# Performance work log

Measured on AMD Instinct MI355X. Metric: run time of the kernel, lower is better.

Reference implementation:

```python
import jax, jax.numpy as jnp
import numpy as np

N, E = 100000, 1280000
IN_D, FEAT, HID, OUT = 256, 64, 64, 64
NEG_SLOPE = 0.2


def _gat_conv(x, src, dst, w, a_s, a_d, b, n):
    # x: [N, in], w: [in, out], a_s/a_d/b: [out]; edges src->dst (messages flow to dst)
    h = x @ w                                   # [N, out]
    e = jax.nn.leaky_relu((h @ a_s)[src] + (h @ a_d)[dst], NEG_SLOPE)  # [E]
    m = jax.ops.segment_max(e, dst, num_segments=n)                     # scatter-softmax (stable)
    ex = jnp.exp(e - m[dst])
    den = jax.ops.segment_sum(ex, dst, num_segments=n)
    alpha = ex / (den[dst] + 1e-16)
    out = jax.ops.segment_sum(alpha[:, None] * h[src], dst, num_segments=n)
    return out + b


def setup_inputs() -> dict:
    key = jax.random.key(0)
    ks = jax.random.split(key, 16)
    rn = lambda k, shape, s=0.05: jax.random.normal(k, shape, jnp.float32) * s
    return {
        'x': jax.random.normal(ks[0], (N, IN_D), jnp.float32),
        'src': jax.random.randint(ks[1], (E,), 0, N),
        'dst': jax.random.randint(ks[2], (E,), 0, N),
        'lin_w': rn(ks[3], (IN_D, FEAT)), 'lin_b': jnp.zeros((FEAT,), jnp.float32),
        'w1': rn(ks[4], (FEAT, HID)), 'a1s': rn(ks[5], (HID,)), 'a1d': rn(ks[6], (HID,)), 'b1': jnp.zeros((HID,), jnp.float32),
        'w2': rn(ks[7], (HID, HID)), 'a2s': rn(ks[8], (HID,)), 'a2d': rn(ks[9], (HID,)), 'b2': jnp.zeros((HID,), jnp.float32),
        'w3': rn(ks[10], (HID, OUT)), 'a3s': rn(ks[11], (OUT,)), 'a3d': rn(ks[12], (OUT,)), 'b3': jnp.zeros((OUT,), jnp.float32),
    }


def reference(x, src, dst, lin_w, lin_b, w1, a1s, a1d, b1, w2, a2s, a2d, b2, w3, a3s, a3d, b3):
    n = x.shape[0]
    loop = jnp.arange(n, dtype=src.dtype)        # GATConv add_self_loops=True
    s = jnp.concatenate([src, loop])
    d = jnp.concatenate([dst, loop])
    h = x @ lin_w + lin_b                        # feature_pre linear
    h = jax.nn.relu(_gat_conv(h, s, d, w1, a1s, a1d, b1, n))  # dropout is identity in eval
    h = jax.nn.relu(_gat_conv(h, s, d, w2, a2s, a2d, b2, n))
    h = _gat_conv(h, s, d, w3, a3s, a3d, b3, n)
    norm = jnp.linalg.norm(h, axis=-1, keepdims=True)          # F.normalize(p=2, dim=-1)
    return h / jnp.maximum(norm, 1e-12)
```

## Files before the change

### kernel.cpp

```cpp
#include <hip/hip_runtime.h>


constexpr float NEG_SLOPE = 0.2f;
#define BKT_SHIFT 9
#define BKT_N     512
#define PCHUNK    2048
#define SRC_BITS  17

typedef __attribute__((ext_vector_type(8))) short bf16x8;
typedef __attribute__((ext_vector_type(4))) float f32x4;

__device__ inline ushort f2bf(float x) {
    union { float f; uint u; } v; v.f = x;
    return (ushort)((v.u + 0x7FFFu + ((v.u >> 16) & 1u)) >> 16);
}
__device__ inline void bf2f(uint u, float& lo, float& hi) {
    union { uint u; float f; } a, b;
    a.u = u << 16; b.u = u & 0xFFFF0000u;
    lo = a.f; hi = b.f;
}
__device__ inline uint pk(float a, float b) {
    return (uint)f2bf(a) | ((uint)f2bf(b) << 16);
}

__global__ __launch_bounds__(256) void prep_w(
    const float* __restrict__ lw, const float* __restrict__ w1,
    const float* __restrict__ w2, const float* __restrict__ w3,
    ushort* __restrict__ lwT, ushort* __restrict__ w1T,
    ushort* __restrict__ w2T, ushort* __restrict__ w3T,
    int* __restrict__ cnt, int* __restrict__ ticket, int n)
{
    const int i = blockIdx.x * 256 + threadIdx.x;
    if (i < n) cnt[i] = 0;
    if (i == 0) *ticket = 0;
    if (i < 64 * 256) {
        const int nn = i >> 8, k = i & 255;
        lwT[i] = f2bf(lw[k * 64 + nn]);
    } else {
        const int j = i - 64 * 256;
        if (j < 4096) {
            const int nn = j >> 6, k = j & 63;
            w1T[j] = f2bf(w1[k * 64 + nn]);
            w2T[j] = f2bf(w2[k * 64 + nn]);
            w3T[j] = f2bf(w3[k * 64 + nn]);
        }
    }
}

__global__ __launch_bounds__(256) void gemm_pre(
    const float* __restrict__ x, const ushort* __restrict__ lwT,
    const float* __restrict__ bias, ushort* __restrict__ C, int M)
{
    __shared__ __align__(16) ushort ctile[4][16][64];
    const int tid = threadIdx.x;
    const int w = tid >> 6, lane = tid & 63;
    const int rw0 = (blockIdx.x * 4 + w) * 16;
    if (rw0 >= M) return;
    const int c = lane & 15, q = lane >> 4;

    const float* ap = x + (size_t)(rw0 + c) * 256 + q * 8;
    float4 pv[16];
    #pragma unroll
    for (int s = 0; s < 8; ++s) {
        pv[2 * s]     = *(const float4*)(ap + s * 32);
        pv[2 * s + 1] = *(const float4*)(ap + s * 32 + 4);
    }

    f32x4 acc[4];
    #pragma unroll
    for (int t = 0; t < 4; ++t) acc[t] = (f32x4){0.f, 0.f, 0.f, 0.f};

    #pragma unroll
    for (int s = 0; s < 8; ++s) {
        const float4 p0 = pv[2 * s];
        const float4 p1 = pv[2 * s + 1];
        bf16x8 af;
        af[0] = (short)f2bf(p0.x); af[1] = (short)f2bf(p0.y);
        af[2] = (short)f2bf(p0.z); af[3] = (short)f2bf(p0.w);
        af[4] = (short)f2bf(p1.x); af[5] = (short)f2bf(p1.y);
        af[6] = (short)f2bf(p1.z); af[7] = (short)f2bf(p1.w);
        #pragma unroll
        for (int t = 0; t < 4; ++t) {
            const bf16x8 bf = *(const bf16x8*)(lwT + (size_t)(t * 16 + c) * 256 + s * 32 + q * 8);
            acc[t] = __builtin_amdgcn_mfma_f32_16x16x32_bf16(af, bf, acc[t], 0, 0, 0);
        }
    }

    #pragma unroll
    for (int t = 0; t < 4; ++t) {
        const float bv = bias[t * 16 + c];
        #pragma unroll
        for (int r = 0; r < 4; ++r)
            ctile[w][q * 4 + r][t * 16 + c] = f2bf(acc[t][r] + bv);
    }
    const int row = lane >> 2, eo = (lane & 3) * 16;
    const uint4 v0 = *(const uint4*)(&ctile[w][row][eo]);
    const uint4 v1 = *(const uint4*)(&ctile[w][row][eo + 8]);
    *(uint4*)(C + (size_t)(rw0 + row) * 64 + eo)     = v0;
    *(uint4*)(C + (size_t)(rw0 + row) * 64 + eo + 8) = v1;
}

__global__ __launch_bounds__(256) void gemm_layer(
    const ushort* __restrict__ A, const ushort* __restrict__ WT,
    const float* __restrict__ a_s, const float* __restrict__ a_d,
    ushort* __restrict__ C, float* __restrict__ hs, float* __restrict__ hd, int M)
{
    __shared__ __align__(16) ushort ctile[4][16][64];
    const int tid = threadIdx.x;
    const int w = tid >> 6, lane = tid & 63;
    const int rw0 = (blockIdx.x * 4 + w) * 16;
    if (rw0 >= M) return;
    const int c = lane & 15, q = lane >> 4;

    const ushort* ap = A + (size_t)(rw0 + c) * 64 + q * 8;
    const bf16x8 a0 = *(const bf16x8*)(ap);
    const bf16x8 a1 = *(const bf16x8*)(ap + 32);

    f32x4 acc[4];
    #pragma unroll
    for (int t = 0; t < 4; ++t) {
        const ushort* bp = WT + (size_t)(t * 16 + c) * 64 + q * 8;
        const bf16x8 b0 = *(const bf16x8*)(bp);
        const bf16x8 b1 = *(const bf16x8*)(bp + 32);
        f32x4 a = (f32x4){0.f, 0.f, 0.f, 0.f};
        a = __builtin_amdgcn_mfma_f32_16x16x32_bf16(a0, b0, a, 0, 0, 0);
        a = __builtin_amdgcn_mfma_f32_16x16x32_bf16(a1, b1, a, 0, 0, 0);
        acc[t] = a;
    }

    float ps[4] = {0.f, 0.f, 0.f, 0.f}, pd[4] = {0.f, 0.f, 0.f, 0.f};
    #pragma unroll
    for (int t = 0; t < 4; ++t) {
        const float as = a_s[t * 16 + c], ad = a_d[t * 16 + c];
        #pragma unroll
        for (int r = 0; r < 4; ++r) {
            ps[r] = fmaf(acc[t][r], as, ps[r]);
            pd[r] = fmaf(acc[t][r], ad, pd[r]);
        }
    }
    #pragma unroll
    for (int r = 0; r < 4; ++r) {
        #pragma unroll
        for (int off = 1; off < 16; off <<= 1) {
            ps[r] += __shfl_xor(ps[r], off);
            pd[r] += __shfl_xor(pd[r], off);
        }
    }
    if (c == 0) {
        #pragma unroll
        for (int r = 0; r < 4; ++r) {
            hs[rw0 + q * 4 + r] = ps[r];
            hd[rw0 + q * 4 + r] = pd[r];
        }
    }

    #pragma unroll
    for (int t = 0; t < 4; ++t)
        #pragma unroll
        for (int r = 0; r < 4; ++r)
            ctile[w][q * 4 + r][t * 16 + c] = f2bf(acc[t][r]);
    const int row = lane >> 2, eo = (lane & 3) * 16;
    const uint4 v0 = *(const uint4*)(&ctile[w][row][eo]);
    const uint4 v1 = *(const uint4*)(&ctile[w][row][eo + 8]);
    *(uint4*)(C + (size_t)(rw0 + row) * 64 + eo)     = v0;
    *(uint4*)(C + (size_t)(rw0 + row) * 64 + eo + 8) = v1;
}

__global__ __launch_bounds__(256) void edge_hist(
    const int* __restrict__ dst, int* __restrict__ cnt, int e)
{
    const int i0 = (blockIdx.x * 256 + threadIdx.x) * 4;
    if (i0 + 3 < e) {
        const int4 d = *(const int4*)(dst + i0);
        atomicAdd(&cnt[d.x], 1); atomicAdd(&cnt[d.y], 1);
        atomicAdd(&cnt[d.z], 1); atomicAdd(&cnt[d.w], 1);
    } else {
        for (int k = i0; k < e; ++k) atomicAdd(&cnt[dst[k]], 1);
    }
}

__global__ __launch_bounds__(256) void scan1(
    const int* __restrict__ cnt, int* __restrict__ out,
    int* __restrict__ bsum, int* __restrict__ ticket, int n, int nblk)
{
    __shared__ int wsum[4];
    __shared__ int amLastS;
    const int tid  = threadIdx.x;
    const int lane = tid & 63;
    const int w    = tid >> 6;
    const int base = blockIdx.x * 1024;
    int vals[4];
    int tsum = 0;
    #pragma unroll
    for (int i = 0; i < 4; ++i) {
        const int idx = base + tid * 4 + i;
        vals[i] = (idx < n) ? cnt[idx] : 0;
        tsum += vals[i];
    }
    int x = tsum;
    #pragma unroll
    for (int off = 1; off < 64; off <<= 1) {
        const int y = __shfl_up(x, off);
        if (lane >= off) x += y;
    }
    if (lane == 63) wsum[w] = x;
    __syncthreads();
    int wofs = 0;
    for (int k = 0; k < w; ++k) wofs += wsum[k];
    int excl = wofs + x - tsum;
    #pragma unroll
    for (int i = 0; i < 4; ++i) {
        const int idx = base + tid * 4 + i;
        if (idx < n) out[idx] = excl;
        excl += vals[i];
    }
    if (tid == 255) {
        bsum[blockIdx.x] = wofs + x;
        __threadfence();
        amLastS = (atomicAdd(ticket, 1) == nblk - 1) ? 1 : 0;
    }
    __syncthreads();
    if (amLastS) {
        __threadfence();
        const int v2 = (tid < nblk) ? bsum[tid] : 0;
        int x2 = v2;
        #pragma unroll
        for (int off = 1; off < 64; off <<= 1) {
            const int y = __shfl_up(x2, off);
            if (lane >= off) x2 += y;
        }
        if (lane == 63) wsum[w] = x2;
        __syncthreads();
        int c2 = 0;
        for (int k = 0; k < w; ++k) c2 += wsum[k];
        if (tid < nblk) bsum[tid] = c2 + x2 - v2;
    }
}

__global__ __launch_bounds__(256) void scan3(
    int* __restrict__ out, const int* __restrict__ bsum,
    int* __restrict__ gcur, int n, int total)
{
    const int idx = blockIdx.x * blockDim.x + threadIdx.x;
    if (idx < n) {
        const int v = out[idx] + bsum[idx >> 10];
        out[idx] = v;
        if ((idx & (BKT_N - 1)) == 0) gcur[idx >> BKT_SHIFT] = v;
    }
    if (idx == 0) out[n] = total;
}

__global__ __launch_bounds__(256) void edge_partition(
    const int* __restrict__ src, const int* __restrict__ dst,
    int* __restrict__ gcursor, int* __restrict__ pairs, int e, int nb)
{
    __shared__ int stage[PCHUNK];
    __shared__ unsigned char sbkt[PCHUNK];
    __shared__ int lcnt[256];
    __shared__ int lstart[256];
    __shared__ int lfill[256];
    __shared__ int gbase[256];
    __shared__ int wsum[4];

    const int tid  = threadIdx.x;
    const int lane = tid & 63;
    const int w    = tid >> 6;
    const int base = blockIdx.x * PCHUNK;
    const int cnt_here = min(PCHUNK, e - base);

    lcnt[tid] = 0; lfill[tid] = 0;
    __syncthreads();

    for (int i = tid; i < cnt_here; i += 256)
        atomicAdd(&lcnt[dst[base + i] >> BKT_SHIFT], 1);
    __syncthreads();

    const int v = lcnt[tid];
    int x = v;
    #pragma unroll
    for (int off = 1; off < 64; off <<= 1) {
        const int y = __shfl_up(x, off);
        if (lane >= off) x += y;
    }
    if (lane == 63) wsum[w] = x;
    __syncthreads();
    int carry = 0;
    for (int k = 0; k < w; ++k) carry += wsum[k];
    lstart[tid] = carry + x - v;
    if (tid < nb && v > 0) gbase[tid] = atomicAdd(&gcursor[tid], v);
    __syncthreads();

    for (int i = tid; i < cnt_here; i += 256) {
        const int d = dst[base + i];
        const int s = src[base + i];
        const int b = d >> BKT_SHIFT;
        const int p = lstart[b] + atomicAdd(&lfill[b], 1);
        stage[p] = ((d & (BKT_N - 1)) << SRC_BITS) | s;
        sbkt[p]  = (unsigned char)b;
    }
    __syncthreads();

    for (int t = tid; t < cnt_here; t += 256) {
        const int b = sbkt[t];
        pairs[gbase[b] + (t - lstart[b])] = stage[t];
    }
}

__global__ __launch_bounds__(256) void bucket_scatter(
    const int* __restrict__ pairs, const int* __restrict__ offs,
    int* __restrict__ ssrc, int n)
{
    __shared__ int pos[BKT_N];
    const int node0 = blockIdx.x << BKT_SHIFT;
    const int node1 = min(n, node0 + BKT_N);
    const int tid = threadIdx.x;
    for (int i = tid; i < node1 - node0; i += 256) pos[i] = offs[node0 + i];
    __syncthreads();
    const int e0 = offs[node0];
    const int e1 = offs[node1];
    for (int j = e0 + tid; j < e1; j += 256) {
        const int pr = pairs[j];
        const int p = atomicAdd(&pos[pr >> SRC_BITS], 1);
        ssrc[p] = pr & ((1 << SRC_BITS) - 1);
    }
}

template <int MODE>
__global__ __launch_bounds__(256) void gat_agg(
    const ushort* __restrict__ hp, const float* __restrict__ hs,
    const float* __restrict__ hd, const int* __restrict__ offs,
    const int* __restrict__ ssrc, const float* __restrict__ bias,
    void* __restrict__ outv, int n)
{
    const int wid  = (blockIdx.x * blockDim.x + threadIdx.x) >> 6;
    const int lane = threadIdx.x & 63;
    if (wid >= n) return;
    const int sub = lane >> 3;
    const int f0  = (lane & 7) * 8;

    const int start = offs[wid];
    const int end   = offs[wid + 1];
    const float hdi = hd[wid];

    int j = start + sub;
    bool vC = j < end;
    bool vN = j + 8 < end;
    int sC = vC ? ssrc[j]     : wid;
    int sN = vN ? ssrc[j + 8] : sC;

    float den = 0.f;
    float acc[8] = {};

    if (sub == 0) {
        const uint4 t = *(const uint4*)(hp + (size_t)wid * 64 + f0);
        float e = hs[wid] + hdi;
        e = (e > 0.f) ? e : NEG_SLOPE * e;
        const float ex = __expf(e);
        float f[8];
        bf2f(t.x, f[0], f[1]); bf2f(t.y, f[2], f[3]);
        bf2f(t.z, f[4], f[5]); bf2f(t.w, f[6], f[7]);
        den = ex;
        #pragma unroll
        for (int i = 0; i < 8; ++i) acc[i] = ex * f[i];
    }

    float hsC = hs[sC];
    uint4 tC  = *(const uint4*)(hp + (size_t)sC * 64 + f0);

    while (vC) {
        const bool vNN = j + 16 < end;
        const int  sNN = vNN ? ssrc[j + 16] : sN;
        const float hsN = hs[sN];
        const uint4 tN  = *(const uint4*)(hp + (size_t)sN * 64 + f0);

        float e2 = hsC + hdi;
        e2 = (e2 > 0.f) ? e2 : NEG_SLOPE * e2;
        const float ex2 = __expf(e2);
        float f[8];
        bf2f(tC.x, f[0], f[1]); bf2f(tC.y, f[2], f[3]);
        bf2f(tC.z, f[4], f[5]); bf2f(tC.w, f[6], f[7]);
        den += ex2;
        #pragma unroll
        for (int i = 0; i < 8; ++i) acc[i] = fmaf(ex2, f[i], acc[i]);

        vC = vN; vN = vNN; sC = sN; sN = sNN; hsC = hsN; tC = tN;
        j += 8;
    }

    #pragma unroll
    for (int off = 8; off < 64; off <<= 1) {
        den += __shfl_xor(den, off);
        #pragma unroll
        for (int i = 0; i < 8; ++i) acc[i] += __shfl_xor(acc[i], off);
    }

    const float4 bv0 = *(const float4*)(bias + f0);
    const float4 bv1 = *(const float4*)(bias + f0 + 4);
    const float bb[8] = {bv0.x, bv0.y, bv0.z, bv0.w, bv1.x, bv1.y, bv1.z, bv1.w};
    const float inv = 1.f / (den + 1e-16f);
    float v[8];
    #pragma unroll
    for (int i = 0; i < 8; ++i) v[i] = acc[i] * inv + bb[i];

    if (MODE == 0) {
        #pragma unroll
        for (int i = 0; i < 8; ++i) v[i] = fmaxf(v[i], 0.f);
        if (sub == 0) {
            uint4 o;
            o.x = pk(v[0], v[1]); o.y = pk(v[2], v[3]);
            o.z = pk(v[4], v[5]); o.w = pk(v[6], v[7]);
            *(uint4*)((ushort*)outv + (size_t)wid * 64 + f0) = o;
        }
    } else {
        float sq = 0.f;
        #pragma unroll
        for (int i = 0; i < 8; ++i) sq += v[i] * v[i];
        #pragma unroll
        for (int off = 1; off < 8; off <<= 1) sq += __shfl_xor(sq, off);
        const float s = 1.f / fmaxf(sqrtf(sq), 1e-12f);
        if (sub == 0) {
            float* op = (float*)outv + (size_t)wid * 64 + f0;
            float4 o0, o1;
            o0.x = v[0] * s; o0.y = v[1] * s; o0.z = v[2] * s; o0.w = v[3] * s;
            o1.x = v[4] * s; o1.y = v[5] * s; o1.z = v[6] * s; o1.w = v[7] * s;
            *(float4*)(op)     = o0;
            *(float4*)(op + 4) = o1;
        }
    }
}

extern "C" void kernel_launch(void* const* d_in, const int* in_sizes, int n_in,
                              void* d_out, int out_size, void* d_ws, size_t ws_size,
                              hipStream_t stream)
{
    const float* x     = (const float*)d_in[0];
    const int*   src   = (const int*)d_in[1];
    const int*   dst   = (const int*)d_in[2];
    const float* lin_w = (const float*)d_in[3];
    const float* lin_b = (const float*)d_in[4];
    const float* w1  = (const float*)d_in[5];
    const float* a1s = (const float*)d_in[6];
    const float* a1d = (const float*)d_in[7];
    const float* b1  = (const float*)d_in[8];
    const float* w2  = (const float*)d_in[9];
    const float* a2s = (const float*)d_in[10];
    const float* a2d = (const float*)d_in[11];
    const float* b2  = (const float*)d_in[12];
    const float* w3  = (const float*)d_in[13];
    const float* a3s = (const float*)d_in[14];
    const float* a3d = (const float*)d_in[15];
    const float* b3  = (const float*)d_in[16];

    const int n = in_sizes[0] / 256;
    const int E = in_sizes[1];
    const int nb = (n + BKT_N - 1) >> BKT_SHIFT;

    char* wsp = (char*)d_ws;
    auto alloc = [&](size_t bytes) -> void* {
        void* p = (void*)wsp;
        wsp += (bytes + 255) & ~(size_t)255;
        return p;
    };
    ushort* bufA = (ushort*)alloc((size_t)n * 64 * sizeof(ushort));
    ushort* bufB = (ushort*)alloc((size_t)n * 64 * sizeof(ushort));
    float*  hs   = (float*)alloc((size_t)n * sizeof(float));
    float*  hd   = (float*)alloc((size_t)n * sizeof(float));
    int*    offs = (int*)alloc((size_t)(n + 1) * sizeof(int));
    int*    cnt  = (int*)alloc((size_t)n * sizeof(int));
    int*    bsum = (int*)alloc(1024 * sizeof(int));
    int*    gcur = (int*)alloc(256 * sizeof(int));
    int*    tick = (int*)alloc(256 * sizeof(int));
    int*    ssrc = (int*)alloc((size_t)E * sizeof(int));
    int*    pairs = (int*)alloc((size_t)E * sizeof(int));
    ushort* lwT = (ushort*)alloc(64 * 256 * sizeof(ushort));
    ushort* w1T = (ushort*)alloc(64 * 64 * sizeof(ushort));
    ushort* w2T = (ushort*)alloc(64 * 64 * sizeof(ushort));
    ushort* w3T = (ushort*)alloc(64 * 64 * sizeof(ushort));

    const int nodeWaveBlocks = (n + 3) / 4;
    const int gemmBlocks = (n + 63) / 64;
    const int nScanBlocks = (n + 1023) / 1024;
    const int partBlocks = (E + PCHUNK - 1) / PCHUNK;
    const int histBlocks = (E / 4 + 255) / 256 + 1;

    prep_w<<<(n + 255) / 256, 256, 0, stream>>>(
        lin_w, w1, w2, w3, lwT, w1T, w2T, w3T, cnt, tick, n);
    edge_hist<<<histBlocks, 256, 0, stream>>>(dst, cnt, E);
    scan1<<<nScanBlocks, 256, 0, stream>>>(cnt, offs, bsum, tick, n, nScanBlocks);
    scan3<<<(n + 255) / 256, 256, 0, stream>>>(offs, bsum, gcur, n, E);
    edge_partition<<<partBlocks, 256, 0, stream>>>(src, dst, gcur, pairs, E, nb);
    bucket_scatter<<<nb, 256, 0, stream>>>(pairs, offs, ssrc, n);

    gemm_pre<<<gemmBlocks, 256, 0, stream>>>(x, lwT, lin_b, bufA, n);

    gemm_layer<<<gemmBlocks, 256, 0, stream>>>(bufA, w1T, a1s, a1d, bufB, hs, hd, n);
    gat_agg<0><<<nodeWaveBlocks, 256, 0, stream>>>(bufB, hs, hd, offs, ssrc, b1, bufA, n);

    gemm_layer<<<gemmBlocks, 256, 0, stream>>>(bufA, w2T, a2s, a2d, bufB, hs, hd, n);
    gat_agg<0><<<nodeWaveBlocks, 256, 0, stream>>>(bufB, hs, hd, offs, ssrc, b2, bufA, n);

    gemm_layer<<<gemmBlocks, 256, 0, stream>>>(bufA, w3T, a3s, a3d, bufB, hs, hd, n);
    gat_agg<1><<<nodeWaveBlocks, 256, 0, stream>>>(bufB, hs, hd, offs, ssrc, b3,
                                                   d_out, n);
}
```

Measured before the change: 490.4 us.

## Replace bucketed CSR build with atomic scatter and overlap input GEMM tiles

Drops the two-pass bucket partition (edge_partition plus bucket_scatter) and builds the CSR source list with one pass of per-edge global atomics on a per-node cursor. The input projection GEMM is split into tiles that run as extra blocks inside the scan and scatter launches, so its memory-bound work shares those launches with the latency-bound CSR steps. The atomic scatter makes the order of edges within each node nondeterministic and sends random writes to global memory. The extra tile blocks can also take compute units away from the scan and scatter blocks.

```diff
diff --git a/kernel.cpp b/kernel.cpp
--- a/kernel.cpp
+++ b/kernel.cpp
@@ -2,10 +2,6 @@
 
 
 constexpr float NEG_SLOPE = 0.2f;
-#define BKT_SHIFT 9
-#define BKT_N     512
-#define PCHUNK    2048
-#define SRC_BITS  17
 
 typedef __attribute__((ext_vector_type(8))) short bf16x8;
 typedef __attribute__((ext_vector_type(4))) float f32x4;
@@ -47,14 +43,14 @@
     }
 }
 
-__global__ __launch_bounds__(256) void gemm_pre(
+__device__ __forceinline__ void gemm_pre_tile(
     const float* __restrict__ x, const ushort* __restrict__ lwT,
-    const float* __restrict__ bias, ushort* __restrict__ C, int M)
+    const float* __restrict__ bias, ushort* __restrict__ C, int M, int tile)
 {
     __shared__ __align__(16) ushort ctile[4][16][64];
     const int tid = threadIdx.x;
     const int w = tid >> 6, lane = tid & 63;
-    const int rw0 = (blockIdx.x * 4 + w) * 16;
+    const int rw0 = (tile * 4 + w) * 16;
     if (rw0 >= M) return;
     const int c = lane & 15, q = lane >> 4;
 
@@ -179,12 +175,18 @@
     }
 }
 
-__global__ __launch_bounds__(256) void scan1(
+__global__ __launch_bounds__(256) void scan1_tiles(
     const int* __restrict__ cnt, int* __restrict__ out,
-    int* __restrict__ bsum, int* __restrict__ ticket, int n, int nblk)
+    int* __restrict__ bsum, int* __restrict__ ticket, int n, int nblk,
+    const float* __restrict__ x, const ushort* __restrict__ lwT,
+    const float* __restrict__ lin_b, ushort* __restrict__ C, int M, int tile0)
 {
     __shared__ int wsum[4];
     __shared__ int amLastS;
+    if ((int)blockIdx.x >= nblk) {
+        gemm_pre_tile(x, lwT, lin_b, C, M, tile0 + (int)blockIdx.x - nblk);
+        return;
+    }
     const int tid  = threadIdx.x;
     const int lane = tid & 63;
     const int w    = tid >> 6;
@@ -197,17 +199,17 @@
         vals[i] = (idx < n) ? cnt[idx] : 0;
         tsum += vals[i];
     }
-    int x = tsum;
+    int x1 = tsum;
     #pragma unroll
     for (int off = 1; off < 64; off <<= 1) {
-        const int y = __shfl_up(x, off);
-        if (lane >= off) x += y;
-    }
-    if (lane == 63) wsum[w] = x;
+        const int y = __shfl_up(x1, off);
+        if (lane >= off) x1 += y;
+    }
+    if (lane == 63) wsum[w] = x1;
     __syncthreads();
     int wofs = 0;
     for (int k = 0; k < w; ++k) wofs += wsum[k];
-    int excl = wofs + x - tsum;
+    int excl = wofs + x1 - tsum;
     #pragma unroll
     for (int i = 0; i < 4; ++i) {
         const int idx = base + tid * 4 + i;
@@ -215,7 +217,7 @@
         excl += vals[i];
     }
     if (tid == 255) {
-        bsum[blockIdx.x] = wofs + x;
+        bsum[blockIdx.x] = wofs + x1;
         __threadfence();
         amLastS = (atomicAdd(ticket, 1) == nblk - 1) ? 1 : 0;
     }
@@ -237,91 +239,49 @@
     }
 }
 
-__global__ __launch_bounds__(256) void scan3(
+__global__ __launch_bounds__(256) void scan3_tiles(
     int* __restrict__ out, const int* __restrict__ bsum,
-    int* __restrict__ gcur, int n, int total)
-{
-    const int idx = blockIdx.x * blockDim.x + threadIdx.x;
+    int* __restrict__ cur, int n, int total, int s3b,
+    const float* __restrict__ x, const ushort* __restrict__ lwT,
+    const float* __restrict__ lin_b, ushort* __restrict__ C, int M, int tile0)
+{
+    if ((int)blockIdx.x >= s3b) {
+        gemm_pre_tile(x, lwT, lin_b, C, M, tile0 + (int)blockIdx.x - s3b);
+        return;
+    }
+    const int idx = blockIdx.x * 256 + threadIdx.x;
     if (idx < n) {
         const int v = out[idx] + bsum[idx >> 10];
         out[idx] = v;
-        if ((idx & (BKT_N - 1)) == 0) gcur[idx >> BKT_SHIFT] = v;
+        cur[idx] = v;
     }
     if (idx == 0) out[n] = total;
 }
 
-__global__ __launch_bounds__(256) void edge_partition(
+__global__ __launch_bounds__(256) void scatter_tiles(
     const int* __restrict__ src, const int* __restrict__ dst,
-    int* __restrict__ gcursor, int* __restrict__ pairs, int e, int nb)
-{
-    __shared__ int stage[PCHUNK];
-    __shared__ unsigned char sbkt[PCHUNK];
-    __shared__ int lcnt[256];
-    __shared__ int lstart[256];
-    __shared__ int lfill[256];
-    __shared__ int gbase[256];
-    __shared__ int wsum[4];
-
-    const int tid  = threadIdx.x;
-    const int lane = tid & 63;
-    const int w    = tid >> 6;
-    const int base = blockIdx.x * PCHUNK;
-    const int cnt_here = min(PCHUNK, e - base);
-
-    lcnt[tid] = 0; lfill[tid] = 0;
-    __syncthreads();
-
-    for (int i = tid; i < cnt_here; i += 256)
-        atomicAdd(&lcnt[dst[base + i] >> BKT_SHIFT], 1);
-    __syncthreads();
-
-    const int v = lcnt[tid];
-    int x = v;
-    #pragma unroll
-    for (int off = 1; off < 64; off <<= 1) {
-        const int y = __shfl_up(x, off);
-        if (lane >= off) x += y;
-    }
-    if (lane == 63) wsum[w] = x;
-    __syncthreads();
-    int carry = 0;
-    for (int k = 0; k < w; ++k) carry += wsum[k];
-    lstart[tid] = carry + x - v;
-    if (tid < nb && v > 0) gbase[tid] = atomicAdd(&gcursor[tid], v);
-    __syncthreads();
-
-    for (int i = tid; i < cnt_here; i += 256) {
-        const int d = dst[base + i];
-        const int s = src[base + i];
-        const int b = d >> BKT_SHIFT;
-        const int p = lstart[b] + atomicAdd(&lfill[b], 1);
-        stage[p] = ((d & (BKT_N - 1)) << SRC_BITS) | s;
-        sbkt[p]  = (unsigned char)b;
-    }
-    __syncthreads();
-
-    for (int t = tid; t < cnt_here; t += 256) {
-        const int b = sbkt[t];
-        pairs[gbase[b] + (t - lstart[b])] = stage[t];
-    }
-}
-
-__global__ __launch_bounds__(256) void bucket_scatter(
-    const int* __restrict__ pairs, const int* __restrict__ offs,
-    int* __restrict__ ssrc, int n)
-{
-    __shared__ int pos[BKT_N];
-    const int node0 = blockIdx.x << BKT_SHIFT;
-    const int node1 = min(n, node0 + BKT_N);
-    const int tid = threadIdx.x;
-    for (int i = tid; i < node1 - node0; i += 256) pos[i] = offs[node0 + i];
-    __syncthreads();
-    const int e0 = offs[node0];
-    const int e1 = offs[node1];
-    for (int j = e0 + tid; j < e1; j += 256) {
-        const int pr = pairs[j];
-        const int p = atomicAdd(&pos[pr >> SRC_BITS], 1);
-        ssrc[p] = pr & ((1 << SRC_BITS) - 1);
+    int* __restrict__ cur, int* __restrict__ ssrc, int e, int sb,
+    const float* __restrict__ x, const ushort* __restrict__ lwT,
+    const float* __restrict__ lin_b, ushort* __restrict__ C, int M, int tile0)
+{
+    if ((int)blockIdx.x >= sb) {
+        gemm_pre_tile(x, lwT, lin_b, C, M, tile0 + (int)blockIdx.x - sb);
+        return;
+    }
+    const int i0 = (blockIdx.x * 256 + threadIdx.x) * 4;
+    if (i0 + 3 < e) {
+        const int4 d = *(const int4*)(dst + i0);
+        const int4 s = *(const int4*)(src + i0);
+        int p;
+        p = atomicAdd(&cur[d.x], 1); ssrc[p] = s.x;
+        p = atomicAdd(&cur[d.y], 1); ssrc[p] = s.y;
+        p = atomicAdd(&cur[d.z], 1); ssrc[p] = s.z;
+        p = atomicAdd(&cur[d.w], 1); ssrc[p] = s.w;
+    } else {
+        for (int k = i0; k < e; ++k) {
+            const int p = atomicAdd(&cur[dst[k]], 1);
+            ssrc[p] = src[k];
+        }
     }
 }
 
@@ -453,7 +413,6 @@
 
     const int n = in_sizes[0] / 256;
     const int E = in_sizes[1];
-    const int nb = (n + BKT_N - 1) >> BKT_SHIFT;
 
     char* wsp = (char*)d_ws;
     auto alloc = [&](size_t bytes) -> void* {
@@ -468,10 +427,8 @@
     int*    offs = (int*)alloc((size_t)(n + 1) * sizeof(int));
     int*    cnt  = (int*)alloc((size_t)n * sizeof(int));
     int*    bsum = (int*)alloc(1024 * sizeof(int));
-    int*    gcur = (int*)alloc(256 * sizeof(int));
     int*    tick = (int*)alloc(256 * sizeof(int));
     int*    ssrc = (int*)alloc((size_t)E * sizeof(int));
-    int*    pairs = (int*)alloc((size_t)E * sizeof(int));
     ushort* lwT = (ushort*)alloc(64 * 256 * sizeof(ushort));
     ushort* w1T = (ushort*)alloc(64 * 64 * sizeof(ushort));
     ushort* w2T = (ushort*)alloc(64 * 64 * sizeof(ushort));
@@ -480,18 +437,26 @@
     const int nodeWaveBlocks = (n + 3) / 4;
     const int gemmBlocks = (n + 63) / 64;
     const int nScanBlocks = (n + 1023) / 1024;
-    const int partBlocks = (E + PCHUNK - 1) / PCHUNK;
+    const int s3Blocks = (n + 255) / 256;
     const int histBlocks = (E / 4 + 255) / 256 + 1;
+    const int scatBlocks = (E / 4 + 255) / 256 + 1;
+
+    const int TA = 256;
+    const int TB = 384;
+    const int TC = gemmBlocks - TA - TB;
 
     prep_w<<<(n + 255) / 256, 256, 0, stream>>>(
         lin_w, w1, w2, w3, lwT, w1T, w2T, w3T, cnt, tick, n);
     edge_hist<<<histBlocks, 256, 0, stream>>>(dst, cnt, E);
-    scan1<<<nScanBlocks, 256, 0, stream>>>(cnt, offs, bsum, tick, n, nScanBlocks);
-    scan3<<<(n + 255) / 256, 256, 0, stream>>>(offs, bsum, gcur, n, E);
-    edge_partition<<<partBlocks, 256, 0, stream>>>(src, dst, gcur, pairs, E, nb);
-    bucket_scatter<<<nb, 256, 0, stream>>>(pairs, offs, ssrc, n);
-
-    gemm_pre<<<gemmBlocks, 256, 0, stream>>>(x, lwT, lin_b, bufA, n);
+    scan1_tiles<<<nScanBlocks + TA, 256, 0, stream>>>(
+        cnt, offs, bsum, tick, n, nScanBlocks,
+        x, lwT, lin_b, bufA, n, 0);
+    scan3_tiles<<<s3Blocks + TB, 256, 0, stream>>>(
+        offs, bsum, cnt, n, E, s3Blocks,
+        x, lwT, lin_b, bufA, n, TA);
+    scatter_tiles<<<scatBlocks + TC, 256, 0, stream>>>(
+        src, dst, cnt, ssrc, E, scatBlocks,
+        x, lwT, lin_b, bufA, n, TA + TB);
 
     gemm_layer<<<gemmBlocks, 256, 0, stream>>>(bufA, w1T, a1s, a1d, bufB, hs, hd, n);
     gat_agg<0><<<nodeWaveBlocks, 256, 0, stream>>>(bufB, hs, hd, offs, ssrc, b1, bufA, n);
```

New measurement: 540.5 us. +10.2%, slower.

## Split input linear GEMM tiles across CSR-build kernels to overlap work

Applied to the files above, without the earlier changes.

Removes the standalone gemm_pre launch and spreads its row tiles across the scan1, scan3, edge_partition and bucket_scatter launches as extra blocks. The latency-bound, low-occupancy CSR-construction kernels then share the GPU with independent GEMM work, and one launch is saved. The cost is larger shared-memory footprints per block, since the GEMM tile's LDS adds to each host kernel's, which may lower occupancy of the graph kernels. The fixed tile split (200/300/400/rest) may also be unbalanced.

```diff
diff --git a/kernel.cpp b/kernel.cpp
--- a/kernel.cpp
+++ b/kernel.cpp
@@ -47,14 +47,14 @@
     }
 }
 
-__global__ __launch_bounds__(256) void gemm_pre(
+__device__ __forceinline__ void gemm_pre_tile(
     const float* __restrict__ x, const ushort* __restrict__ lwT,
-    const float* __restrict__ bias, ushort* __restrict__ C, int M)
+    const float* __restrict__ bias, ushort* __restrict__ C, int M, int tile)
 {
     __shared__ __align__(16) ushort ctile[4][16][64];
     const int tid = threadIdx.x;
     const int w = tid >> 6, lane = tid & 63;
-    const int rw0 = (blockIdx.x * 4 + w) * 16;
+    const int rw0 = (tile * 4 + w) * 16;
     if (rw0 >= M) return;
     const int c = lane & 15, q = lane >> 4;
 
@@ -179,12 +179,18 @@
     }
 }
 
-__global__ __launch_bounds__(256) void scan1(
+__global__ __launch_bounds__(256) void scan1_tiles(
     const int* __restrict__ cnt, int* __restrict__ out,
-    int* __restrict__ bsum, int* __restrict__ ticket, int n, int nblk)
+    int* __restrict__ bsum, int* __restrict__ ticket, int n, int nblk,
+    const float* __restrict__ x, const ushort* __restrict__ lwT,
+    const float* __restrict__ lin_b, ushort* __restrict__ C, int M, int tile0)
 {
     __shared__ int wsum[4];
     __shared__ int amLastS;
+    if ((int)blockIdx.x >= nblk) {
+        gemm_pre_tile(x, lwT, lin_b, C, M, tile0 + (int)blockIdx.x - nblk);
+        return;
+    }
     const int tid  = threadIdx.x;
     const int lane = tid & 63;
     const int w    = tid >> 6;
@@ -197,17 +203,17 @@
         vals[i] = (idx < n) ? cnt[idx] : 0;
         tsum += vals[i];
     }
-    int x = tsum;
+    int x1 = tsum;
     #pragma unroll
     for (int off = 1; off < 64; off <<= 1) {
-        const int y = __shfl_up(x, off);
-        if (lane >= off) x += y;
-    }
-    if (lane == 63) wsum[w] = x;
+        const int y = __shfl_up(x1, off);
+        if (lane >= off) x1 += y;
+    }
+    if (lane == 63) wsum[w] = x1;
     __syncthreads();
     int wofs = 0;
     for (int k = 0; k < w; ++k) wofs += wsum[k];
-    int excl = wofs + x - tsum;
+    int excl = wofs + x1 - tsum;
     #pragma unroll
     for (int i = 0; i < 4; ++i) {
         const int idx = base + tid * 4 + i;
@@ -215,7 +221,7 @@
         excl += vals[i];
     }
     if (tid == 255) {
-        bsum[blockIdx.x] = wofs + x;
+        bsum[blockIdx.x] = wofs + x1;
         __threadfence();
         amLastS = (atomicAdd(ticket, 1) == nblk - 1) ? 1 : 0;
     }
@@ -237,11 +243,17 @@
     }
 }
 
-__global__ __launch_bounds__(256) void scan3(
+__global__ __launch_bounds__(256) void scan3_tiles(
     int* __restrict__ out, const int* __restrict__ bsum,
-    int* __restrict__ gcur, int n, int total)
-{
-    const int idx = blockIdx.x * blockDim.x + threadIdx.x;
+    int* __restrict__ gcur, int n, int total, int s3b,
+    const float* __restrict__ x, const ushort* __restrict__ lwT,
+    const float* __restrict__ lin_b, ushort* __restrict__ C, int M, int tile0)
+{
+    if ((int)blockIdx.x >= s3b) {
+        gemm_pre_tile(x, lwT, lin_b, C, M, tile0 + (int)blockIdx.x - s3b);
+        return;
+    }
+    const int idx = blockIdx.x * 256 + threadIdx.x;
     if (idx < n) {
         const int v = out[idx] + bsum[idx >> 10];
         out[idx] = v;
@@ -250,9 +262,11 @@
     if (idx == 0) out[n] = total;
 }
 
-__global__ __launch_bounds__(256) void edge_partition(
+__global__ __launch_bounds__(256) void part_tiles(
     const int* __restrict__ src, const int* __restrict__ dst,
-    int* __restrict__ gcursor, int* __restrict__ pairs, int e, int nb)
+    int* __restrict__ gcursor, int* __restrict__ pairs, int e, int nb, int pb,
+    const float* __restrict__ x, const ushort* __restrict__ lwT,
+    const float* __restrict__ lin_b, ushort* __restrict__ C, int M, int tile0)
 {
     __shared__ int stage[PCHUNK];
     __shared__ unsigned char sbkt[PCHUNK];
@@ -262,6 +276,11 @@
     __shared__ int gbase[256];
     __shared__ int wsum[4];
 
+    if ((int)blockIdx.x >= pb) {
+        gemm_pre_tile(x, lwT, lin_b, C, M, tile0 + (int)blockIdx.x - pb);
+        return;
+    }
+
     const int tid  = threadIdx.x;
     const int lane = tid & 63;
     const int w    = tid >> 6;
@@ -276,17 +295,17 @@
     __syncthreads();
 
     const int v = lcnt[tid];
-    int x = v;
+    int x1 = v;
     #pragma unroll
     for (int off = 1; off < 64; off <<= 1) {
-        const int y = __shfl_up(x, off);
-        if (lane >= off) x += y;
-    }
-    if (lane == 63) wsum[w] = x;
+        const int y = __shfl_up(x1, off);
+        if (lane >= off) x1 += y;
+    }
+    if (lane == 63) wsum[w] = x1;
     __syncthreads();
     int carry = 0;
     for (int k = 0; k < w; ++k) carry += wsum[k];
-    lstart[tid] = carry + x - v;
+    lstart[tid] = carry + x1 - v;
     if (tid < nb && v > 0) gbase[tid] = atomicAdd(&gcursor[tid], v);
     __syncthreads();
 
@@ -306,11 +325,17 @@
     }
 }
 
-__global__ __launch_bounds__(256) void bucket_scatter(
+__global__ __launch_bounds__(256) void scat_tiles(
     const int* __restrict__ pairs, const int* __restrict__ offs,
-    int* __restrict__ ssrc, int n)
+    int* __restrict__ ssrc, int n, int sb,
+    const float* __restrict__ x, const ushort* __restrict__ lwT,
+    const float* __restrict__ lin_b, ushort* __restrict__ C, int M, int tile0)
 {
     __shared__ int pos[BKT_N];
+    if ((int)blockIdx.x >= sb) {
+        gemm_pre_tile(x, lwT, lin_b, C, M, tile0 + (int)blockIdx.x - sb);
+        return;
+    }
     const int node0 = blockIdx.x << BKT_SHIFT;
     const int node1 = min(n, node0 + BKT_N);
     const int tid = threadIdx.x;
@@ -480,18 +505,30 @@
     const int nodeWaveBlocks = (n + 3) / 4;
     const int gemmBlocks = (n + 63) / 64;
     const int nScanBlocks = (n + 1023) / 1024;
+    const int s3Blocks = (n + 255) / 256;
+    const int histBlocks = (E / 4 + 255) / 256 + 1;
     const int partBlocks = (E + PCHUNK - 1) / PCHUNK;
-    const int histBlocks = (E / 4 + 255) / 256 + 1;
+
+    const int TA = 200;
+    const int TB = 300;
+    const int TC = 400;
+    const int TD = gemmBlocks - TA - TB - TC;
 
     prep_w<<<(n + 255) / 256, 256, 0, stream>>>(
         lin_w, w1, w2, w3, lwT, w1T, w2T, w3T, cnt, tick, n);
     edge_hist<<<histBlocks, 256, 0, stream>>>(dst, cnt, E);
-    scan1<<<nScanBlocks, 256, 0, stream>>>(cnt, offs, bsum, tick, n, nScanBlocks);
-    scan3<<<(n + 255) / 256, 256, 0, stream>>>(offs, bsum, gcur, n, E);
-    edge_partition<<<partBlocks, 256, 0, stream>>>(src, dst, gcur, pairs, E, nb);
-    bucket_scatter<<<nb, 256, 0, stream>>>(pairs, offs, ssrc, n);
-
-    gemm_pre<<<gemmBlocks, 256, 0, stream>>>(x, lwT, lin_b, bufA, n);
+    scan1_tiles<<<nScanBlocks + TA, 256, 0, stream>>>(
+        cnt, offs, bsum, tick, n, nScanBlocks,
+        x, lwT, lin_b, bufA, n, 0);
+    scan3_tiles<<<s3Blocks + TB, 256, 0, stream>>>(
+        offs, bsum, gcur, n, E, s3Blocks,
+        x, lwT, lin_b, bufA, n, TA);
+    part_tiles<<<partBlocks + TC, 256, 0, stream>>>(
+        src, dst, gcur, pairs, E, nb, partBlocks,
+        x, lwT, lin_b, bufA, n, TA + TB);
+    scat_tiles<<<nb + TD, 256, 0, stream>>>(
+        pairs, offs, ssrc, n, nb,
+        x, lwT, lin_b, bufA, n, TA + TB + TC);
 
     gemm_layer<<<gemmBlocks, 256, 0, stream>>>(bufA, w1T, a1s, a1d, bufB, hs, hd, n);
     gat_agg<0><<<nodeWaveBlocks, 256, 0, stream>>>(bufB, hs, hd, offs, ssrc, b1, bufA, n);
```

Measured after the change: 497.0 us. Within noise of the previous version (+1.3%).
